# Performance work log

Hardware: AMD Instinct MI355X
Metric: run time of the kernel (lower is better)

The kernel has to match this reference:

```python
import jax, jax.numpy as jnp
import numpy as np

N = 200000   # active voxels
K = 27       # 3x3x3 kernel volume
CIN = 32
COUT = 64


def setup_inputs() -> dict:
    key = jax.random.key(0)
    k1, k2, k3, k4 = jax.random.split(key, 4)
    features = jax.random.normal(k1, (N, CIN), dtype=jnp.float32)
    # kernel map: for each kernel offset k and output voxel n, index of the
    # contributing input voxel (or masked out if that neighbor is inactive)
    neighbor_map = jax.random.randint(k2, (K, N), 0, N, dtype=jnp.int32)
    neighbor_mask = jax.random.randint(k3, (K, N), 0, 2) > 0
    std = 1.0 / float(np.sqrt(CIN * K))  # matches reset_parameters
    kernel = jax.random.uniform(k4, (K, CIN, COUT), dtype=jnp.float32,
                                minval=-std, maxval=std)
    return {"features": features, "neighbor_map": neighbor_map,
            "neighbor_mask": neighbor_mask, "kernel": kernel}


def reference(features, neighbor_map, neighbor_mask, kernel):
    # Sparse conv3d as gather -> per-offset matmul -> accumulate.
    # scan over the K=27 kernel offsets keeps peak memory at one gathered
    # [N, CIN] buffer instead of materializing [K, N, CIN].
    n_out = features.shape[0]
    cout = kernel.shape[-1]

    def body(acc, inp):
        nm_k, mask_k, w_k = inp  # [N], [N], [CIN, COUT]
        g = features[nm_k] * mask_k[:, None].astype(features.dtype)  # gather [N, CIN]
        return acc + g @ w_k, None

    init = jnp.zeros((n_out, cout), dtype=features.dtype)
    out, _ = jax.lax.scan(body, init, (neighbor_map, neighbor_mask, kernel))
    return out
```

## Files before the change

### kernel.cpp

```cpp
#include <hip/hip_runtime.h>

#define CIN   32
#define COUT  64
#define K_OFF 27

typedef __attribute__((ext_vector_type(8))) short bf16x8;
typedef __attribute__((ext_vector_type(4))) float f32x4;

#define FENCE_VM(N) asm volatile("s_waitcnt vmcnt(" #N ")" ::: "memory")
#define PIN()       asm volatile("" ::: "memory")

__device__ inline unsigned short f2bf_rne(float f) {
    union { float f; unsigned int u; } v; v.f = f;
    unsigned int u = v.u;
    u = (u + 0x7fffu + ((u >> 16) & 1u)) >> 16;
    return (unsigned short)u;
}

__device__ inline void async_load16(const void* g, void* l) {
    __builtin_amdgcn_global_load_lds(
        (const __attribute__((address_space(1))) void*)g,
        (__attribute__((address_space(3))) void*)l, 16, 0, 0);
}

__global__ __launch_bounds__(256) void detect_mask(
    const unsigned char* __restrict__ mask, int nbytes, int* __restrict__ flag,
    float* __restrict__ zrow) {
    __shared__ int wany[4];
    int found = 0;
    for (int i = threadIdx.x; i < nbytes; i += 256)
        if ((i & 3) && mask[i]) found = 1;
    unsigned long long b = __ballot(found);
    if ((threadIdx.x & 63) == 0) wany[threadIdx.x >> 6] = b ? 1 : 0;
    __syncthreads();
    if (threadIdx.x == 0) *flag = wany[0] | wany[1] | wany[2] | wany[3];
    if (threadIdx.x < 16) zrow[threadIdx.x] = 0.0f;
}

__global__ __launch_bounds__(256) void prep_kernel(
    const float* __restrict__ feat, const int* __restrict__ nmap,
    const unsigned char* __restrict__ mask8, const int* __restrict__ mask32,
    const float* __restrict__ wk,
    unsigned short* __restrict__ featb, int* __restrict__ midx,
    unsigned short* __restrict__ wt2,
    int n, int Bf, int Bm, const int* __restrict__ flag)
{
    const int gid = blockIdx.x;
    if (gid < Bf) {
        const int base = (gid * 256 + threadIdx.x) * 8;
        if (base < n * CIN) {
            float4 a = *(const float4*)(feat + base);
            float4 b = *(const float4*)(feat + base + 4);
            bf16x8 v;
            v[0] = (short)f2bf_rne(a.x); v[1] = (short)f2bf_rne(a.y);
            v[2] = (short)f2bf_rne(a.z); v[3] = (short)f2bf_rne(a.w);
            v[4] = (short)f2bf_rne(b.x); v[5] = (short)f2bf_rne(b.y);
            v[6] = (short)f2bf_rne(b.z); v[7] = (short)f2bf_rne(b.w);
            *(bf16x8*)(featb + base) = v;
        }
    } else if (gid < Bf + Bm) {
        const int t = (gid - Bf) * 256 + threadIdx.x;
        int i = t * 4;
        const int total = K_OFF * n;
        const int is_b8 = *flag;
        if (i + 3 < total) {
            int4 nm = *(const int4*)(nmap + i);
            int m0, m1, m2, m3;
            if (is_b8) {
                uchar4 mb = *(const uchar4*)(mask8 + i);
                m0 = mb.x; m1 = mb.y; m2 = mb.z; m3 = mb.w;
            } else {
                int4 mm = *(const int4*)(mask32 + i);
                m0 = mm.x; m1 = mm.y; m2 = mm.z; m3 = mm.w;
            }
            int4 r;
            r.x = m0 ? nm.x : -1; r.y = m1 ? nm.y : -1;
            r.z = m2 ? nm.z : -1; r.w = m3 ? nm.w : -1;
            *(int4*)(midx + i) = r;
        } else {
            for (; i < total; ++i) {
                int m = is_b8 ? (int)mask8[i] : mask32[i];
                midx[i] = m ? nmap[i] : -1;
            }
        }
    } else {
        const int t = (gid - Bf - Bm) * 256 + threadIdx.x;
        if (t < K_OFF * 4 * 64) {
            const int lane = t & 63, ct = (t >> 6) & 3, k = t >> 8;
            const int lrow = lane & 15, q = lane >> 4;
            const int col = ct * 16 + lrow;
            bf16x8 v;
            #pragma unroll
            for (int j = 0; j < 8; ++j)
                v[j] = (short)f2bf_rne(wk[(k * CIN + q * 8 + j) * COUT + col]);
            *(bf16x8*)(wt2 + t * 8) = v;
        }
    }
}

__global__ __launch_bounds__(256) void conv_mfma9(
    const unsigned short* __restrict__ featb,
    const int*            __restrict__ midx,
    const unsigned short* __restrict__ wt2,
    const unsigned short* __restrict__ zrow,
    float* __restrict__ out, int n)
{
    __shared__ __attribute__((aligned(16))) unsigned short As0[4][2][512];
    __shared__ __attribute__((aligned(16))) unsigned short As1[4][2][512];
    __shared__ __attribute__((aligned(16))) unsigned short As2[4][2][512];
    __shared__ __attribute__((aligned(16))) unsigned short As3[4][2][512];

    const int tid  = threadIdx.x;
    const int wave = tid >> 6;
    const int lane = tid & 63;
    const int lrow = lane & 15;
    const int q    = lane >> 4;
    const int n0   = blockIdx.x * 128 + wave * 32;

    const int  row0 = n0 + lrow, row1 = n0 + 16 + lrow;
    const bool vr0 = row0 < n, vr1 = row1 < n;

    auto load_mi = [&](int k, int rt) -> int {
        const int  r = rt ? row1 : row0;
        const bool v = rt ? vr1 : vr0;
        if (!v) return -1;
        return midx[k * n + r];
    };
    auto slotp = [&](int s, int rt) -> unsigned short* {
        return s == 0 ? &As0[wave][rt][0]
             : s == 1 ? &As1[wave][rt][0]
             : s == 2 ? &As2[wave][rt][0]
                      : &As3[wave][rt][0];
    };
    auto issue_gather = [&](int mi, unsigned short* ldsbase) {
        const unsigned short* src =
            (mi >= 0) ? featb + (size_t)mi * CIN + q * 8 : zrow;
        async_load16(src, ldsbase);
    };
    auto loadB = [&](int k, bf16x8* dst) {
        const unsigned short* p = wt2 + ((k * 4) << 9) + lane * 8;
        #pragma unroll
        for (int ct = 0; ct < 4; ++ct) dst[ct] = *(const bf16x8*)(p + (ct << 9));
    };

    int    mi_buf[2][2];
    bf16x8 B_buf[2][4];
    f32x4  acc[2][4] = {};

    {
        int p00 = load_mi(0, 0), p01 = load_mi(0, 1);
        int p10 = load_mi(1, 0), p11 = load_mi(1, 1);
        int p20 = load_mi(2, 0), p21 = load_mi(2, 1);
        mi_buf[1][0] = load_mi(3, 0);
        mi_buf[1][1] = load_mi(3, 1);
        PIN();
        issue_gather(p00, slotp(0, 0)); issue_gather(p01, slotp(0, 1));
        PIN();
        issue_gather(p10, slotp(1, 0)); issue_gather(p11, slotp(1, 1));
        PIN();
        issue_gather(p20, slotp(2, 0)); issue_gather(p21, slotp(2, 1));
        PIN();
        loadB(0, B_buf[0]);
        PIN();
    }

    #pragma unroll
    for (int k = 0; k < K_OFF; ++k) {
        if      (k == 0)  FENCE_VM(8);
        else if (k == 1)  FENCE_VM(14);
        else if (k <= 23) FENCE_VM(20);
        else if (k == 24) FENCE_VM(18);
        else if (k == 25) FENCE_VM(14);
        else              FENCE_VM(12);

        bf16x8 a0 = *(const bf16x8*)(slotp(k & 3, 0) + lane * 8);
        bf16x8 a1 = *(const bf16x8*)(slotp(k & 3, 1) + lane * 8);

        if (k + 4 < K_OFF) {
            mi_buf[k & 1][0] = load_mi(k + 4, 0);
            mi_buf[k & 1][1] = load_mi(k + 4, 1);
        }
        PIN();
        if (k + 3 < K_OFF) {
            issue_gather(mi_buf[(k + 1) & 1][0], slotp((k + 3) & 3, 0));
            issue_gather(mi_buf[(k + 1) & 1][1], slotp((k + 3) & 3, 1));
        }
        PIN();
        if (k + 1 < K_OFF) loadB(k + 1, B_buf[(k + 1) & 1]);
        PIN();

        const int bs = k & 1;
        #pragma unroll
        for (int ct = 0; ct < 4; ++ct) {
            acc[0][ct] = __builtin_amdgcn_mfma_f32_16x16x32_bf16(
                a0, B_buf[bs][ct], acc[0][ct], 0, 0, 0);
            acc[1][ct] = __builtin_amdgcn_mfma_f32_16x16x32_bf16(
                a1, B_buf[bs][ct], acc[1][ct], 0, 0, 0);
        }
    }

    #pragma unroll
    for (int rt = 0; rt < 2; ++rt)
        #pragma unroll
        for (int ct = 0; ct < 4; ++ct)
            #pragma unroll
            for (int r = 0; r < 4; ++r) {
                const int row = n0 + rt * 16 + q * 4 + r;
                if (row < n) out[(size_t)row * COUT + ct * 16 + lrow] = acc[rt][ct][r];
            }
}

#define BN 64
__global__ __launch_bounds__(256) void sparse_conv_fp32(
    const float* __restrict__ feat, const int* __restrict__ nmap,
    const unsigned char* __restrict__ mask8, const int* __restrict__ mask32,
    const float* __restrict__ wk, float* __restrict__ out,
    int n, const int* __restrict__ flag)
{
    __shared__ float A[CIN][BN];
    __shared__ float W[CIN][COUT];
    const int tid = threadIdx.x;
    const int n0 = blockIdx.x * BN;
    const int is_b8 = *flag;
    const int r0 = (tid >> 4) * 4, c0 = (tid & 15) * 4;
    const int grow = tid >> 2, gpart = tid & 3;
    float acc[4][4] = {};
    for (int k = 0; k < K_OFF; ++k) {
        {
            const int base = tid * 8;
            const float* wsrc = wk + (size_t)k * (CIN * COUT) + base;
            float4 w0 = ((const float4*)wsrc)[0];
            float4 w1 = ((const float4*)wsrc)[1];
            *(float4*)&W[base >> 6][base & 63] = w0;
            *(float4*)&W[base >> 6][(base & 63) + 4] = w1;
        }
        {
            const int gn = n0 + grow;
            float4 f0 = make_float4(0.f, 0.f, 0.f, 0.f), f1 = f0;
            if (gn < n) {
                const int idx = k * n + gn;
                const int m = is_b8 ? (int)mask8[idx] : mask32[idx];
                if (m) {
                    const float* fsrc = feat + (size_t)nmap[idx] * CIN + gpart * 8;
                    f0 = ((const float4*)fsrc)[0];
                    f1 = ((const float4*)fsrc)[1];
                }
            }
            const int cb = gpart * 8;
            A[cb+0][grow]=f0.x; A[cb+1][grow]=f0.y; A[cb+2][grow]=f0.z; A[cb+3][grow]=f0.w;
            A[cb+4][grow]=f1.x; A[cb+5][grow]=f1.y; A[cb+6][grow]=f1.z; A[cb+7][grow]=f1.w;
        }
        __syncthreads();
        #pragma unroll
        for (int c = 0; c < CIN; ++c) {
            const float4 a = *(const float4*)&A[c][r0];
            const float4 w = *(const float4*)&W[c][c0];
            acc[0][0]+=a.x*w.x; acc[0][1]+=a.x*w.y; acc[0][2]+=a.x*w.z; acc[0][3]+=a.x*w.w;
            acc[1][0]+=a.y*w.x; acc[1][1]+=a.y*w.y; acc[1][2]+=a.y*w.z; acc[1][3]+=a.y*w.w;
            acc[2][0]+=a.z*w.x; acc[2][1]+=a.z*w.y; acc[2][2]+=a.z*w.z; acc[2][3]+=a.z*w.w;
            acc[3][0]+=a.w*w.x; acc[3][1]+=a.w*w.y; acc[3][2]+=a.w*w.z; acc[3][3]+=a.w*w.w;
        }
        __syncthreads();
    }
    #pragma unroll
    for (int i = 0; i < 4; ++i) {
        const int orow = n0 + r0 + i;
        if (orow < n)
            *(float4*)&out[(size_t)orow * COUT + c0] =
                make_float4(acc[i][0], acc[i][1], acc[i][2], acc[i][3]);
    }
}

static inline size_t align16(size_t x) { return (x + 15) & ~(size_t)15; }

extern "C" void kernel_launch(void* const* d_in, const int* in_sizes, int n_in,
                              void* d_out, int out_size, void* d_ws, size_t ws_size,
                              hipStream_t stream) {
    const float*         feat = (const float*)d_in[0];
    const int*           nmap = (const int*)d_in[1];
    const unsigned char* m8   = (const unsigned char*)d_in[2];
    const int*           m32  = (const int*)d_in[2];
    const float*         wk   = (const float*)d_in[3];
    float*               out  = (float*)d_out;

    const int n = in_sizes[0] / CIN;
    int* flag = (int*)d_ws;
    float* zrow = (float*)((char*)d_ws + 64);

    const size_t feat_off   = 128;
    const size_t feat_bytes = (size_t)n * CIN * 2;
    const size_t midx_off   = align16(feat_off + feat_bytes);
    const size_t midx_bytes = (size_t)K_OFF * n * 4;
    const size_t wt2_off    = align16(midx_off + midx_bytes);
    const size_t wt2_bytes  = (size_t)K_OFF * 4 * 64 * 8 * 2;
    const size_t needed     = wt2_off + wt2_bytes;

    const int mask_elems = K_OFF * n;
    const int det_bytes  = mask_elems < 4096 ? mask_elems : 4096;
    detect_mask<<<1, 256, 0, stream>>>(m8, det_bytes, flag, zrow);

    if (ws_size >= needed) {
        unsigned short* featb = (unsigned short*)((char*)d_ws + feat_off);
        int*            midx  = (int*)((char*)d_ws + midx_off);
        unsigned short* wt2   = (unsigned short*)((char*)d_ws + wt2_off);
        const int Bf = (n * CIN / 8 + 255) / 256;
        const int Bm = ((K_OFF * n + 3) / 4 + 255) / 256;
        const int Bw = (K_OFF * 4 * 64 + 255) / 256;
        prep_kernel<<<Bf + Bm + Bw, 256, 0, stream>>>(
            feat, nmap, m8, m32, wk, featb, midx, wt2, n, Bf, Bm, flag);
        const int nblocks = (n + 127) / 128;
        conv_mfma9<<<nblocks, 256, 0, stream>>>(
            featb, midx, wt2, (const unsigned short*)zrow, out, n);
    } else {
        const int nb = (n + BN - 1) / BN;
        sparse_conv_fp32<<<nb, 256, 0, stream>>>(feat, nmap, m8, m32, wk, out, n, flag);
    }
}
```

Baseline: 178.0 us.

## Stage weights cooperatively in LDS with triple-buffered pipeline and block barriers

Weight tiles were loaded by every wave straight into registers. Now each wave async-loads one quarter of the per-offset weight tile into shared LDS, and all waves read it from there. The A gather buffers move from four-deep to a three-deep ring with prefetch distance 2, synchronised by vmcnt waits plus an s_barrier per offset. This cuts redundant global weight traffic and register pressure, at the cost of a block-wide barrier every iteration and a shallower gather prefetch.

```diff
diff --git a/kernel.cpp b/kernel.cpp
--- a/kernel.cpp
+++ b/kernel.cpp
@@ -9,6 +9,7 @@
 
 #define FENCE_VM(N) asm volatile("s_waitcnt vmcnt(" #N ")" ::: "memory")
 #define PIN()       asm volatile("" ::: "memory")
+#define BARRIER()   asm volatile("s_barrier" ::: "memory")
 
 __device__ inline unsigned short f2bf_rne(float f) {
     union { float f; unsigned int u; } v; v.f = f;
@@ -98,17 +99,15 @@
     }
 }
 
-__global__ __launch_bounds__(256) void conv_mfma9(
+__global__ __launch_bounds__(256) void conv_mfma10(
     const unsigned short* __restrict__ featb,
     const int*            __restrict__ midx,
     const unsigned short* __restrict__ wt2,
     const unsigned short* __restrict__ zrow,
     float* __restrict__ out, int n)
 {
-    __shared__ __attribute__((aligned(16))) unsigned short As0[4][2][512];
-    __shared__ __attribute__((aligned(16))) unsigned short As1[4][2][512];
-    __shared__ __attribute__((aligned(16))) unsigned short As2[4][2][512];
-    __shared__ __attribute__((aligned(16))) unsigned short As3[4][2][512];
+    __shared__ __attribute__((aligned(16))) unsigned short Bs[3][4][512];
+    __shared__ __attribute__((aligned(16))) unsigned short As[3][4][2][512];
 
     const int tid  = threadIdx.x;
     const int wave = tid >> 6;
@@ -126,76 +125,77 @@
         if (!v) return -1;
         return midx[k * n + r];
     };
-    auto slotp = [&](int s, int rt) -> unsigned short* {
-        return s == 0 ? &As0[wave][rt][0]
-             : s == 1 ? &As1[wave][rt][0]
-             : s == 2 ? &As2[wave][rt][0]
-                      : &As3[wave][rt][0];
-    };
     auto issue_gather = [&](int mi, unsigned short* ldsbase) {
         const unsigned short* src =
             (mi >= 0) ? featb + (size_t)mi * CIN + q * 8 : zrow;
         async_load16(src, ldsbase);
     };
-    auto loadB = [&](int k, bf16x8* dst) {
-        const unsigned short* p = wt2 + ((k * 4) << 9) + lane * 8;
-        #pragma unroll
-        for (int ct = 0; ct < 4; ++ct) dst[ct] = *(const bf16x8*)(p + (ct << 9));
+    auto stageB = [&](int k) {
+        const unsigned short* src = wt2 + (((k * 4 + wave)) << 9) + lane * 8;
+        async_load16(src, &Bs[k % 3][wave][0]);
     };
 
-    int    mi_buf[2][2];
-    bf16x8 B_buf[2][4];
-    f32x4  acc[2][4] = {};
+    int   mi_buf[2][2];
+    f32x4 acc[2][4] = {};
 
     {
         int p00 = load_mi(0, 0), p01 = load_mi(0, 1);
         int p10 = load_mi(1, 0), p11 = load_mi(1, 1);
-        int p20 = load_mi(2, 0), p21 = load_mi(2, 1);
-        mi_buf[1][0] = load_mi(3, 0);
-        mi_buf[1][1] = load_mi(3, 1);
-        PIN();
-        issue_gather(p00, slotp(0, 0)); issue_gather(p01, slotp(0, 1));
-        PIN();
-        issue_gather(p10, slotp(1, 0)); issue_gather(p11, slotp(1, 1));
-        PIN();
-        issue_gather(p20, slotp(2, 0)); issue_gather(p21, slotp(2, 1));
-        PIN();
-        loadB(0, B_buf[0]);
-        PIN();
+        mi_buf[0][0] = load_mi(2, 0); mi_buf[0][1] = load_mi(2, 1);
+        mi_buf[1][0] = load_mi(3, 0); mi_buf[1][1] = load_mi(3, 1);
+        PIN();
+        stageB(0);
+        stageB(1);
+        PIN();
+        issue_gather(p00, &As[0][wave][0][0]);
+        issue_gather(p01, &As[0][wave][1][0]);
+        PIN();
+        issue_gather(p10, &As[1][wave][0][0]);
+        issue_gather(p11, &As[1][wave][1][0]);
+        PIN();
+        FENCE_VM(2);
+        BARRIER();
     }
 
     #pragma unroll
     for (int k = 0; k < K_OFF; ++k) {
-        if      (k == 0)  FENCE_VM(8);
-        else if (k == 1)  FENCE_VM(14);
-        else if (k <= 23) FENCE_VM(20);
-        else if (k == 24) FENCE_VM(18);
-        else if (k == 25) FENCE_VM(14);
-        else              FENCE_VM(12);
-
-        bf16x8 a0 = *(const bf16x8*)(slotp(k & 3, 0) + lane * 8);
-        bf16x8 a1 = *(const bf16x8*)(slotp(k & 3, 1) + lane * 8);
-
+        bf16x8 a0 = *(const bf16x8*)(&As[k % 3][wave][0][lane * 8]);
+        bf16x8 a1 = *(const bf16x8*)(&As[k % 3][wave][1][lane * 8]);
+        bf16x8 b0 = *(const bf16x8*)(&Bs[k % 3][0][lane * 8]);
+        bf16x8 b1 = *(const bf16x8*)(&Bs[k % 3][1][lane * 8]);
+        bf16x8 b2 = *(const bf16x8*)(&Bs[k % 3][2][lane * 8]);
+        bf16x8 b3 = *(const bf16x8*)(&Bs[k % 3][3][lane * 8]);
+        PIN();
+
+        if (k + 2 < K_OFF) {
+            stageB(k + 2);
+            PIN();
+            issue_gather(mi_buf[k & 1][0], &As[(k + 2) % 3][wave][0][0]);
+            issue_gather(mi_buf[k & 1][1], &As[(k + 2) % 3][wave][1][0]);
+            PIN();
+        }
         if (k + 4 < K_OFF) {
             mi_buf[k & 1][0] = load_mi(k + 4, 0);
             mi_buf[k & 1][1] = load_mi(k + 4, 1);
-        }
-        PIN();
-        if (k + 3 < K_OFF) {
-            issue_gather(mi_buf[(k + 1) & 1][0], slotp((k + 3) & 3, 0));
-            issue_gather(mi_buf[(k + 1) & 1][1], slotp((k + 3) & 3, 1));
-        }
-        PIN();
-        if (k + 1 < K_OFF) loadB(k + 1, B_buf[(k + 1) & 1]);
-        PIN();
-
-        const int bs = k & 1;
-        #pragma unroll
-        for (int ct = 0; ct < 4; ++ct) {
-            acc[0][ct] = __builtin_amdgcn_mfma_f32_16x16x32_bf16(
-                a0, B_buf[bs][ct], acc[0][ct], 0, 0, 0);
-            acc[1][ct] = __builtin_amdgcn_mfma_f32_16x16x32_bf16(
-                a1, B_buf[bs][ct], acc[1][ct], 0, 0, 0);
+            PIN();
+        }
+
+        acc[0][0] = __builtin_amdgcn_mfma_f32_16x16x32_bf16(a0, b0, acc[0][0], 0, 0, 0);
+        acc[1][0] = __builtin_amdgcn_mfma_f32_16x16x32_bf16(a1, b0, acc[1][0], 0, 0, 0);
+        acc[0][1] = __builtin_amdgcn_mfma_f32_16x16x32_bf16(a0, b1, acc[0][1], 0, 0, 0);
+        acc[1][1] = __builtin_amdgcn_mfma_f32_16x16x32_bf16(a1, b1, acc[1][1], 0, 0, 0);
+        acc[0][2] = __builtin_amdgcn_mfma_f32_16x16x32_bf16(a0, b2, acc[0][2], 0, 0, 0);
+        acc[1][2] = __builtin_amdgcn_mfma_f32_16x16x32_bf16(a1, b2, acc[1][2], 0, 0, 0);
+        acc[0][3] = __builtin_amdgcn_mfma_f32_16x16x32_bf16(a0, b3, acc[0][3], 0, 0, 0);
+        acc[1][3] = __builtin_amdgcn_mfma_f32_16x16x32_bf16(a1, b3, acc[1][3], 0, 0, 0);
+
+        if (k < K_OFF - 1) {
+            if      (k == 0)  FENCE_VM(5);
+            else if (k <= 22) FENCE_VM(7);
+            else if (k == 23) FENCE_VM(5);
+            else if (k == 24) FENCE_VM(3);
+            else              FENCE_VM(0);
+            BARRIER();
         }
     }
 
@@ -309,7 +309,7 @@
         prep_kernel<<<Bf + Bm + Bw, 256, 0, stream>>>(
             feat, nmap, m8, m32, wk, featb, midx, wt2, n, Bf, Bm, flag);
         const int nblocks = (n + 127) / 128;
-        conv_mfma9<<<nblocks, 256, 0, stream>>>(
+        conv_mfma10<<<nblocks, 256, 0, stream>>>(
             featb, midx, wt2, (const unsigned short*)zrow, out, n);
     } else {
         const int nb = (n + BN - 1) / BN;
```

New measurement: 169.9 us. 1.05x faster.
